# Optimization experiments

Measured on AMD Instinct MI355X. Metric: run time of the kernel, lower is better.

The kernel has to match this reference:

```python
import jax, jax.numpy as jnp
import numpy as np

NEG_SLOPE = 0.2

def gatv2_layer(x, src, dst, Wl, bl, Wr, br, att, bias, N, concat):
    # Wl/Wr: [F_in, H*C]; att: [H, C]
    H, C = att.shape
    xl = (x @ Wl + bl).reshape(-1, H, C)  # source transform [N,H,C]
    xr = (x @ Wr + br).reshape(-1, H, C)  # target transform [N,H,C]
    e = jax.nn.leaky_relu(xl[src] + xr[dst], NEG_SLOPE)          # [E,H,C]
    logits = jnp.einsum('ehc,hc->eh', e, att)                    # [E,H]
    m = jax.ops.segment_max(logits, dst, num_segments=N)         # [N,H]
    p = jnp.exp(logits - m[dst])
    s = jax.ops.segment_sum(p, dst, num_segments=N)              # [N,H]
    alpha = p / s[dst]                                           # [E,H] softmax per dst
    out = jax.ops.segment_sum(alpha[:, :, None] * xl[src], dst, num_segments=N)  # [N,H,C]
    out = out.reshape(N, H * C) if concat else out.mean(axis=1)
    return out + bias


def setup_inputs() -> dict:
    key = jax.random.key(0)
    N, E, F_in = 50000, 500000, 58
    ks = jax.random.split(key, 16)
    s = 0.1
    inp = {
        'x': jax.random.normal(ks[0], (N, F_in), jnp.float32),
        'edge_index': jax.random.randint(ks[1], (2, E), 0, N, jnp.int64),
        'Wl1': jax.random.normal(ks[2], (F_in, 256), jnp.float32) * s,
        'bl1': jnp.zeros((256,), jnp.float32),
        'Wr1': jax.random.normal(ks[3], (F_in, 256), jnp.float32) * s,
        'br1': jnp.zeros((256,), jnp.float32),
        'att1': jax.random.normal(ks[4], (4, 64), jnp.float32) * s,
        'bias1': jnp.zeros((256,), jnp.float32),
        'Wl2': jax.random.normal(ks[5], (256, 256), jnp.float32) * s,
        'bl2': jnp.zeros((256,), jnp.float32),
        'Wr2': jax.random.normal(ks[6], (256, 256), jnp.float32) * s,
        'br2': jnp.zeros((256,), jnp.float32),
        'att2': jax.random.normal(ks[7], (4, 64), jnp.float32) * s,
        'bias2': jnp.zeros((256,), jnp.float32),
        'Wl3': jax.random.normal(ks[8], (256, 6), jnp.float32) * s,
        'bl3': jnp.zeros((6,), jnp.float32),
        'Wr3': jax.random.normal(ks[9], (256, 6), jnp.float32) * s,
        'br3': jnp.zeros((6,), jnp.float32),
        'att3': jax.random.normal(ks[10], (6, 1), jnp.float32) * s,
        'bias3': jnp.zeros((1,), jnp.float32),
    }
    return inp


def reference(x, edge_index, Wl1, bl1, Wr1, br1, att1, bias1,
              Wl2, bl2, Wr2, br2, att2, bias2,
              Wl3, bl3, Wr3, br3, att3, bias3):
    N = x.shape[0]
    loop = jnp.arange(N, dtype=edge_index.dtype)
    src = jnp.concatenate([edge_index[0], loop])  # self-loops (PyG default)
    dst = jnp.concatenate([edge_index[1], loop])
    h = jax.nn.elu(gatv2_layer(x, src, dst, Wl1, bl1, Wr1, br1, att1, bias1, N, True))
    h = jax.nn.elu(gatv2_layer(h, src, dst, Wl2, bl2, Wr2, br2, att2, bias2, N, True))
    out = gatv2_layer(h, src, dst, Wl3, bl3, Wr3, br3, att3, bias3, N, False)
    return out  # [N, 1]
```

## Files before the change

### kernel.cpp

```cpp
#include <hip/hip_runtime.h>
#include <math.h>

#define NEG_SLOPE 0.2f
#define LOG2E 1.4426950408889634f

typedef __attribute__((ext_vector_type(2))) _Float16 h2;
typedef __attribute__((ext_vector_type(4))) _Float16 h4;
typedef __attribute__((ext_vector_type(8))) _Float16 f16x8;
typedef __attribute__((ext_vector_type(4))) float f32x4;

typedef const __attribute__((address_space(1))) unsigned int* gu32p;
typedef __attribute__((address_space(3))) unsigned int* lu32p;

#define GLD16(g, l) __builtin_amdgcn_global_load_lds((gu32p)(g), (lu32p)(l), 16, 0, 0)

template<int CTRL>
__device__ __forceinline__ float dpp_add_f32(float x) {
    int y = __builtin_amdgcn_update_dpp(0, __float_as_int(x), CTRL, 0xF, 0xF, true);
    return x + __int_as_float(y);
}
__device__ __forceinline__ float rowsum16(float x) {
    x = dpp_add_f32<0xB1>(x);
    x = dpp_add_f32<0x4E>(x);
    x = dpp_add_f32<0x124>(x);
    x = dpp_add_f32<0x128>(x);
    return x;
}


__global__ __launch_bounds__(256) void k_scan_block(const int* __restrict__ cnt,
                                                    int* __restrict__ out,
                                                    int* __restrict__ bsums, int n) {
    __shared__ int tmp[256];
    int t = threadIdx.x;
    int i = blockIdx.x * 256 + t;
    int v = (i < n) ? cnt[i] : 0;
    tmp[t] = v;
    __syncthreads();
    for (int d = 1; d < 256; d <<= 1) {
        int add = (t >= d) ? tmp[t - d] : 0;
        __syncthreads();
        tmp[t] += add;
        __syncthreads();
    }
    if (i < n) out[i] = tmp[t] - v;
    if (t == 255) bsums[blockIdx.x] = tmp[t];
}

__global__ __launch_bounds__(256) void k_scan_add(int* __restrict__ out,
                                                  const int* __restrict__ bsums,
                                                  int n, int total, int nb) {
    __shared__ int tmp[256];
    int t = threadIdx.x;
    int v = (t < nb) ? bsums[t] : 0;
    tmp[t] = v;
    __syncthreads();
    for (int d = 1; d < 256; d <<= 1) {
        int add = (t >= d) ? tmp[t - d] : 0;
        __syncthreads();
        tmp[t] += add;
        __syncthreads();
    }
    int boff = tmp[blockIdx.x] - bsums[blockIdx.x];
    int i = blockIdx.x * 256 + t;
    if (i < n) out[i] += boff;
    if (i == 0) out[n] = total;
}


__global__ __launch_bounds__(256) void k_prep(
        const int* __restrict__ ei, int E, int Et, int* __restrict__ cnt,
        int* __restrict__ rank,
        const float* __restrict__ x, _Float16* __restrict__ xb, int N, int F,
        const float* __restrict__ Wl1, const float* __restrict__ Wr1,
        const float* __restrict__ Wl2, const float* __restrict__ Wr2,
        const float* __restrict__ Wl3, const float* __restrict__ Wr3,
        _Float16* __restrict__ wtl1, _Float16* __restrict__ wtr1,
        _Float16* __restrict__ wtl2, _Float16* __restrict__ wtr2,
        _Float16* __restrict__ w3t, int gEt, int gX) {
    const int b = blockIdx.x;
    if (b < gEt) {
        int e = b * 256 + threadIdx.x;
        if (e < Et) {
            int d = (e < E) ? ei[E + e] : (e - E);
            rank[e] = atomicAdd(&cnt[d], 1);
        }
    } else if (b < gEt + gX) {
        int i = (b - gEt) * 256 + threadIdx.x;
        if (i < (N << 6)) {
            int n = i >> 6, k = i & 63;
            xb[i] = (_Float16)(k < F ? x[n * F + k] : 0.0f);
        }
    } else {
        int i = (b - gEt - gX) * 256 + threadIdx.x;
        if (i < 32768) {
            const float* W = (i < 16384) ? Wl1 : Wr1;
            _Float16* O = (i < 16384) ? wtl1 : wtr1;
            int loc = i & 16383;
            int n = loc >> 6, k = loc & 63;
            O[loc] = (_Float16)(k < F ? W[k * 256 + n] : 0.0f);
        } else if (i < 163840) {
            int seg = i - 32768;
            const float* W = (seg < 65536) ? Wl2 : Wr2;
            _Float16* O = (seg < 65536) ? wtl2 : wtr2;
            int loc = seg & 65535;
            int n = loc >> 8, k = loc & 255;
            O[loc] = (_Float16)W[k * 256 + n];
        } else if (i < 167936) {
            int loc = i - 163840;
            int j = loc >> 8, k = loc & 255;
            float v = (j < 6) ? Wl3[k * 6 + j] : ((j < 12) ? Wr3[k * 6 + (j - 6)] : 0.0f);
            w3t[loc] = (_Float16)v;
        }
    }
}


__global__ __launch_bounds__(512) void k_gemm_pair_mfma(
        const _Float16* __restrict__ A, int M, int Kp,
        const _Float16* __restrict__ Btl, const _Float16* __restrict__ Btr,
        const float* __restrict__ bl, const float* __restrict__ br,
        _Float16* __restrict__ Cl, _Float16* __restrict__ Cr,
        const int* __restrict__ ei, int E, int Et,
        const int* __restrict__ row_ptr, const int* __restrict__ rank,
        int* __restrict__ src_sorted,
        int sB, int gX) {
    __shared__ _Float16 As[128 * 32];
    __shared__ _Float16 Bs[256 * 32];
    if (blockIdx.x < sB) {
        int e = blockIdx.x * 512 + threadIdx.x;
        if (e < Et) {
            int s, d;
            if (e < E) { s = ei[e]; d = ei[E + e]; } else { s = d = e - E; }
            src_sorted[row_ptr[d] + rank[e]] = s;
        }
        return;
    }
    const int gb = blockIdx.x - sB;
    const int mat = gb >= gX;
    const int bx  = mat ? gb - gX : gb;
    const int tid = threadIdx.x;
    const int wv = tid >> 6, lane = tid & 63;
    const int wr = wv >> 2, wc = wv & 3;
    const int l15 = lane & 15, l4 = lane >> 4;
    const int row0 = bx * 128;
    const _Float16* Bt = mat ? Btr : Btl;
    const float* bias  = mat ? br  : bl;
    _Float16* C        = mat ? Cr  : Cl;

    const int sr = tid >> 2;
    const int sk = (tid & 3) * 8;
    const _Float16* gA  = A  + (size_t)min(row0 + sr, M - 1) * Kp + sk;
    const _Float16* gB0 = Bt + (size_t)sr * Kp + sk;
    const _Float16* gB1 = Bt + (size_t)(sr + 128) * Kp + sk;
    _Float16* lA  = &As[(wv * 16) * 32];
    _Float16* lB0 = &Bs[(wv * 16) * 32];
    _Float16* lB1 = &Bs[(wv * 16 + 128) * 32];

    f32x4 acc[4][4];
    #pragma unroll
    for (int a = 0; a < 4; a++)
        #pragma unroll
        for (int b = 0; b < 4; b++)
            acc[a][b] = (f32x4){0.f, 0.f, 0.f, 0.f};

    for (int k0 = 0; k0 < Kp; k0 += 32) {
        GLD16(gA + k0, lA);
        GLD16(gB0 + k0, lB0);
        GLD16(gB1 + k0, lB1);
        __syncthreads();
        f16x8 wf[4], xf[4];
        #pragma unroll
        for (int ct = 0; ct < 4; ct++)
            wf[ct] = *(const f16x8*)&Bs[(wc * 64 + ct * 16 + l15) * 32 + l4 * 8];
        #pragma unroll
        for (int nt = 0; nt < 4; nt++)
            xf[nt] = *(const f16x8*)&As[(wr * 64 + nt * 16 + l15) * 32 + l4 * 8];
        #pragma unroll
        for (int ct = 0; ct < 4; ct++)
            #pragma unroll
            for (int nt = 0; nt < 4; nt++)
                acc[ct][nt] = __builtin_amdgcn_mfma_f32_16x16x32_f16(
                    wf[ct], xf[nt], acc[ct][nt], 0, 0, 0);
        __syncthreads();
    }

    float4 bv[4];
    #pragma unroll
    for (int ct = 0; ct < 4; ct++)
        bv[ct] = *(const float4*)&bias[wc * 64 + ct * 16 + l4 * 4];
    #pragma unroll
    for (int nt = 0; nt < 4; nt++) {
        int node = row0 + wr * 64 + nt * 16 + l15;
        if (node < M) {
            #pragma unroll
            for (int ct = 0; ct < 4; ct++) {
                h4 hv = {(_Float16)(acc[ct][nt][0] + bv[ct].x),
                         (_Float16)(acc[ct][nt][1] + bv[ct].y),
                         (_Float16)(acc[ct][nt][2] + bv[ct].z),
                         (_Float16)(acc[ct][nt][3] + bv[ct].w)};
                *(h4*)&C[(size_t)node * 256 + wc * 64 + ct * 16 + l4 * 4] = hv;
            }
        }
    }
}


__global__ __launch_bounds__(256) void k_gemm3_mfma(
        const _Float16* __restrict__ h,
        const _Float16* __restrict__ W3t,
        const float* __restrict__ bl, const float* __restrict__ br,
        _Float16* __restrict__ l3, int N) {
    const int wave = threadIdx.x >> 6, lane = threadIdx.x & 63;
    const int l15 = lane & 15, l4 = lane >> 4;
    const int row0 = blockIdx.x * 64 + wave * 16;
    if (row0 >= N) return;

    f16x8 bfr[8];
    #pragma unroll
    for (int ks = 0; ks < 8; ks++)
        bfr[ks] = *(const f16x8*)&W3t[l15 * 256 + ks * 32 + l4 * 8];

    const int arow = min(row0 + l15, N - 1);
    const size_t abase = (size_t)arow * 256;
    f32x4 acc = (f32x4){0.f, 0.f, 0.f, 0.f};
    #pragma unroll
    for (int ks = 0; ks < 8; ks++) {
        f16x8 af = *(const f16x8*)&h[abase + ks * 32 + l4 * 8];
        acc = __builtin_amdgcn_mfma_f32_16x16x32_f16(af, bfr[ks], acc, 0, 0, 0);
    }
    const float bv = (l15 < 6) ? bl[l15] : ((l15 < 12) ? br[l15 - 6] : 0.0f);
    #pragma unroll
    for (int r = 0; r < 4; r++) {
        int gr = row0 + l4 * 4 + r;
        if (gr < N && l15 < 12)
            l3[(size_t)gr * 16 + l15] = (_Float16)(acc[r] + bv);
    }
}


__global__ __launch_bounds__(256) void k_agg256(const _Float16* __restrict__ xl,
                                                const _Float16* __restrict__ xr,
                                                const int* __restrict__ row_ptr,
                                                const int* __restrict__ src_sorted,
                                                const float* __restrict__ att,
                                                const float* __restrict__ bias,
                                                _Float16* __restrict__ h_out, int N) {
    const int wave = threadIdx.x >> 6;
    const int lane = threadIdx.x & 63;
    const int n = __builtin_amdgcn_readfirstlane(blockIdx.x * 4 + wave);
    if (n >= N) return;
    const int ci = lane * 4;
    const h4 xr4 = *(const h4*)&xr[(size_t)n * 256 + ci];
    const float4 at4 = *(const float4*)&att[ci];
    const h2 ata = {(_Float16)(at4.x * LOG2E), (_Float16)(at4.y * LOG2E)};
    const h2 atb = {(_Float16)(at4.z * LOG2E), (_Float16)(at4.w * LOG2E)};
    h4 a4 = {(_Float16)0.f, (_Float16)0.f, (_Float16)0.f, (_Float16)0.f};
    float m = -INFINITY, s = 0.0f;
    const int beg = row_ptr[n], end = row_ptr[n + 1];
    const int rem = (end - beg) & 7;
    const int tb  = end - rem;

    h4 vt[7];
    #pragma unroll
    for (int e = 0; e < 7; e++) {
        if (e < rem) {
            int sv = src_sorted[tb + e];
            vt[e] = *(const h4*)&xl[(size_t)sv * 256 + ci];
        }
    }

    int j = beg;
    h4 v[8], vn[8];
    bool has = (j + 8 <= tb);
    if (has) {
        #pragma unroll
        for (int e = 0; e < 8; e++) {
            int sv = src_sorted[j + e];
            v[e] = *(const h4*)&xl[(size_t)sv * 256 + ci];
        }
    }
    while (has) {
        const int jn = j + 8;
        const bool hasN = (jn + 8 <= tb);
        if (hasN) {
            #pragma unroll
            for (int e = 0; e < 8; e++) {
                int sv = src_sorted[jn + e];
                vn[e] = *(const h4*)&xl[(size_t)sv * 256 + ci];
            }
        }
        float lg[8];
        #pragma unroll
        for (int e = 0; e < 8; e++) {
            h4 t = v[e] + xr4;
            h4 lk = __builtin_elementwise_max(t, t * (_Float16)NEG_SLOPE);
            h2 lo = __builtin_shufflevector(lk, lk, 0, 1);
            h2 hi = __builtin_shufflevector(lk, lk, 2, 3);
            lg[e] = __builtin_amdgcn_fdot2(lo, ata,
                        __builtin_amdgcn_fdot2(hi, atb, 0.0f, false), false);
        }
        #pragma unroll
        for (int e = 0; e < 8; e++) lg[e] = rowsum16(lg[e]);
        float bm = fmaxf(fmaxf(fmaxf(lg[0], lg[1]), fmaxf(lg[2], lg[3])),
                         fmaxf(fmaxf(lg[4], lg[5]), fmaxf(lg[6], lg[7])));
        float nm = fmaxf(m, bm);
        float sc = __builtin_amdgcn_exp2f(m - nm);
        {
            _Float16 sc16 = (_Float16)sc;
            a4 *= (h4){sc16, sc16, sc16, sc16};
        }
        float ps = 0.f;
        #pragma unroll
        for (int e = 0; e < 8; e++) {
            float p = __builtin_amdgcn_exp2f(lg[e] - nm);
            ps += p;
            _Float16 p16 = (_Float16)p;
            a4 = __builtin_elementwise_fma((h4){p16, p16, p16, p16}, v[e], a4);
        }
        s = s * sc + ps;
        m = nm;
        if (hasN) {
            #pragma unroll
            for (int e = 0; e < 8; e++) v[e] = vn[e];
        }
        j = jn;
        has = hasN;
    }

    if (rem) {
        float lg[7];
        #pragma unroll
        for (int e = 0; e < 7; e++) {
            if (e < rem) {
                h4 t = vt[e] + xr4;
                h4 lk = __builtin_elementwise_max(t, t * (_Float16)NEG_SLOPE);
                h2 lo = __builtin_shufflevector(lk, lk, 0, 1);
                h2 hi = __builtin_shufflevector(lk, lk, 2, 3);
                float d = __builtin_amdgcn_fdot2(lo, ata,
                              __builtin_amdgcn_fdot2(hi, atb, 0.0f, false), false);
                lg[e] = rowsum16(d);
            }
        }
        float bm = -INFINITY;
        #pragma unroll
        for (int e = 0; e < 7; e++)
            if (e < rem) bm = fmaxf(bm, lg[e]);
        float nm = fmaxf(m, bm);
        float sc = __builtin_amdgcn_exp2f(m - nm);
        {
            _Float16 sc16 = (_Float16)sc;
            a4 *= (h4){sc16, sc16, sc16, sc16};
        }
        float ps = 0.f;
        #pragma unroll
        for (int e = 0; e < 7; e++) {
            if (e < rem) {
                float p = __builtin_amdgcn_exp2f(lg[e] - nm);
                ps += p;
                _Float16 p16 = (_Float16)p;
                a4 = __builtin_elementwise_fma((h4){p16, p16, p16, p16}, vt[e], a4);
            }
        }
        s = s * sc + ps;
        m = nm;
    }

    const float inv = 1.0f / s;
    const float4 bv = *(const float4*)&bias[ci];
    float o0 = (float)a4.x * inv + bv.x;
    float o1 = (float)a4.y * inv + bv.y;
    float o2 = (float)a4.z * inv + bv.z;
    float o3 = (float)a4.w * inv + bv.w;
    o0 = o0 > 0.f ? o0 : (__expf(o0) - 1.f);
    o1 = o1 > 0.f ? o1 : (__expf(o1) - 1.f);
    o2 = o2 > 0.f ? o2 : (__expf(o2) - 1.f);
    o3 = o3 > 0.f ? o3 : (__expf(o3) - 1.f);
    h4 hv = {(_Float16)o0, (_Float16)o1, (_Float16)o2, (_Float16)o3};
    *(h4*)&h_out[(size_t)n * 256 + ci] = hv;
}


__global__ __launch_bounds__(256) void k_agg3(const _Float16* __restrict__ l3,
                                              const int* __restrict__ row_ptr,
                                              const int* __restrict__ src_sorted,
                                              const float* __restrict__ att3,
                                              const float* __restrict__ bias3,
                                              float* __restrict__ out, int N) {
    const int idx = blockIdx.x * 256 + threadIdx.x;
    const int n = idx >> 3, h = idx & 7;
    if (n >= N) return;
    float val = 0.0f;
    if (h < 6) {
        const float xrv = (float)l3[(size_t)n * 16 + 6 + h];
        const float attv = att3[h] * LOG2E;
        float m = -INFINITY, s = 0.0f, acc = 0.0f;
        const int beg = row_ptr[n], end = row_ptr[n + 1];
        for (int j = beg; j < end; j += 8) {
            float xlv[8];
            #pragma unroll
            for (int e = 0; e < 8; e++) {
                int i2 = j + e; i2 = i2 < end ? i2 : end - 1;
                int sv = src_sorted[i2];
                xlv[e] = (float)l3[(size_t)sv * 16 + h];
            }
            #pragma unroll
            for (int e = 0; e < 8; e++) {
                const bool valid = (j + e) < end;
                float tt = xlv[e] + xrv;
                float lr = fmaxf(tt, NEG_SLOPE * tt);
                float logit = valid ? (attv * lr) : -INFINITY;
                float nm = fmaxf(m, logit);
                float sc = __builtin_amdgcn_exp2f(m - nm);
                float p  = __builtin_amdgcn_exp2f(logit - nm);
                acc = acc * sc + p * xlv[e];
                s   = s * sc + p;
                m   = nm;
            }
        }
        val = acc / s;
    }
    val += __shfl_xor(val, 1);
    val += __shfl_xor(val, 2);
    val += __shfl_xor(val, 4);
    if (h == 0) out[n] = val * (1.0f / 6.0f) + bias3[0];
}


extern "C" void kernel_launch(void* const* d_in, const int* in_sizes, int n_in,
                              void* d_out, int out_size, void* d_ws, size_t ws_size,
                              hipStream_t stream) {
    const float* x    = (const float*)d_in[0];
    const int*   ei   = (const int*)  d_in[1];
    const float* Wl1  = (const float*)d_in[2];
    const float* bl1  = (const float*)d_in[3];
    const float* Wr1  = (const float*)d_in[4];
    const float* br1  = (const float*)d_in[5];
    const float* att1 = (const float*)d_in[6];
    const float* bias1= (const float*)d_in[7];
    const float* Wl2  = (const float*)d_in[8];
    const float* bl2  = (const float*)d_in[9];
    const float* Wr2  = (const float*)d_in[10];
    const float* br2  = (const float*)d_in[11];
    const float* att2 = (const float*)d_in[12];
    const float* bias2= (const float*)d_in[13];
    const float* Wl3  = (const float*)d_in[14];
    const float* bl3  = (const float*)d_in[15];
    const float* Wr3  = (const float*)d_in[16];
    const float* br3  = (const float*)d_in[17];
    const float* att3 = (const float*)d_in[18];
    const float* bias3= (const float*)d_in[19];

    const int F  = in_sizes[2] / 256;
    const int N  = in_sizes[0] / F;
    const int E  = in_sizes[1] / 2;
    const int Et = E + N;

    char* ws = (char*)d_ws;
    size_t off = 0;
    auto carve = [&](size_t bytes) -> char* {
        char* p = ws + off;
        off = (off + bytes + 255) & ~(size_t)255;
        return p;
    };
    _Float16* xb   = (_Float16*)carve((size_t)N * 64 * 2);
    _Float16* xlb  = (_Float16*)carve((size_t)N * 256 * 2);
    _Float16* xrb  = (_Float16*)carve((size_t)N * 256 * 2);
    _Float16* hb   = (_Float16*)carve((size_t)N * 256 * 2);
    _Float16* wtl1 = (_Float16*)carve(256 * 64 * 2);
    _Float16* wtr1 = (_Float16*)carve(256 * 64 * 2);
    _Float16* wtl2 = (_Float16*)carve(256 * 256 * 2);
    _Float16* wtr2 = (_Float16*)carve(256 * 256 * 2);
    _Float16* w3t  = (_Float16*)carve(16 * 256 * 2);
    _Float16* l3   = (_Float16*)carve((size_t)N * 16 * 2);
    int* cnt        = (int*)carve((size_t)N * 4);
    int* row_ptr    = (int*)carve((size_t)(N + 1) * 4);
    int* rank       = (int*)carve((size_t)Et * 4);
    int* src_sorted = (int*)carve((size_t)Et * 4);
    int* bsums      = (int*)carve(1024 * 4);

    const int gN  = (N + 255) / 256;
    const int gEt = (Et + 255) / 256;
    const int gX  = ((N << 6) + 255) / 256;
    const int gW  = (N + 3) / 4;
    const int gx1 = (N + 127) / 128;
    const int sB  = (Et + 511) / 512;

    hipMemsetAsync(cnt, 0, (size_t)N * 4, stream);
    k_prep<<<gEt + gX + 656, 256, 0, stream>>>(ei, E, Et, cnt, rank, x, xb, N, F,
                                               Wl1, Wr1, Wl2, Wr2, Wl3, Wr3,
                                               wtl1, wtr1, wtl2, wtr2, w3t, gEt, gX);

    k_scan_block<<<gN, 256, 0, stream>>>(cnt, row_ptr, bsums, N);
    k_scan_add<<<gN, 256, 0, stream>>>(row_ptr, bsums, N, Et, gN);

    k_gemm_pair_mfma<<<sB + 2 * gx1, 512, 0, stream>>>(
        xb, N, 64, wtl1, wtr1, bl1, br1, xlb, xrb,
        ei, E, Et, row_ptr, rank, src_sorted, sB, gx1);
    k_agg256<<<gW, 256, 0, stream>>>(xlb, xrb, row_ptr, src_sorted, att1, bias1, hb, N);

    k_gemm_pair_mfma<<<2 * gx1, 512, 0, stream>>>(
        hb, N, 256, wtl2, wtr2, bl2, br2, xlb, xrb,
        ei, E, Et, row_ptr, rank, src_sorted, 0, gx1);
    k_agg256<<<gW, 256, 0, stream>>>(xlb, xrb, row_ptr, src_sorted, att2, bias2, hb, N);

    k_gemm3_mfma<<<(N + 63) / 64, 256, 0, stream>>>(hb, w3t, bl3, br3, l3, N);
    k_agg3<<<((N * 8) + 255) / 256, 256, 0, stream>>>(l3, row_ptr, src_sorted, att3, bias3,
                                                      (float*)d_out, N);
}
```

Baseline: 296.8 us.

## Fuse left and right GEMMs into one 1024-thread block sharing the A tile

The paired GEMM kernel now computes both the Wl and Wr projections in a single 1024-thread block, with waves 0-7 handling the left matrix and waves 8-15 the right. Each shared A tile is loaded once and reused for both outputs, halving A traffic and halving the grid size. The edge-scatter prologue blocks are resized to 1024 threads to match. The cost is that a larger block under launch bounds of 1024 limits registers per thread and lowers scheduling flexibility, and LDS per block grows.

```diff
diff --git a/kernel.cpp b/kernel.cpp
--- a/kernel.cpp
+++ b/kernel.cpp
@@ -116,7 +116,7 @@
 }
 
 
-__global__ __launch_bounds__(512) void k_gemm_pair_mfma(
+__global__ __launch_bounds__(1024) void k_gemm_pair_mfma(
         const _Float16* __restrict__ A, int M, int Kp,
         const _Float16* __restrict__ Btl, const _Float16* __restrict__ Btr,
         const float* __restrict__ bl, const float* __restrict__ br,
@@ -124,11 +124,12 @@
         const int* __restrict__ ei, int E, int Et,
         const int* __restrict__ row_ptr, const int* __restrict__ rank,
         int* __restrict__ src_sorted,
-        int sB, int gX) {
-    __shared__ _Float16 As[128 * 32];
-    __shared__ _Float16 Bs[256 * 32];
+        int sB) {
+    __shared__ _Float16 As [128 * 32];
+    __shared__ _Float16 Bs0[256 * 32];
+    __shared__ _Float16 Bs1[256 * 32];
     if (blockIdx.x < sB) {
-        int e = blockIdx.x * 512 + threadIdx.x;
+        int e = blockIdx.x * 1024 + threadIdx.x;
         if (e < Et) {
             int s, d;
             if (e < E) { s = ei[e]; d = ei[E + e]; } else { s = d = e - E; }
@@ -136,26 +137,26 @@
         }
         return;
     }
-    const int gb = blockIdx.x - sB;
-    const int mat = gb >= gX;
-    const int bx  = mat ? gb - gX : gb;
+    const int bx  = blockIdx.x - sB;
     const int tid = threadIdx.x;
     const int wv = tid >> 6, lane = tid & 63;
-    const int wr = wv >> 2, wc = wv & 3;
+    const int mat = wv >> 3;
+    const int wq  = wv & 7;
+    const int wr = wq >> 2, wc = wq & 3;
     const int l15 = lane & 15, l4 = lane >> 4;
     const int row0 = bx * 128;
-    const _Float16* Bt = mat ? Btr : Btl;
     const float* bias  = mat ? br  : bl;
     _Float16* C        = mat ? Cr  : Cl;
 
     const int sr = tid >> 2;
     const int sk = (tid & 3) * 8;
-    const _Float16* gA  = A  + (size_t)min(row0 + sr, M - 1) * Kp + sk;
-    const _Float16* gB0 = Bt + (size_t)sr * Kp + sk;
-    const _Float16* gB1 = Bt + (size_t)(sr + 128) * Kp + sk;
-    _Float16* lA  = &As[(wv * 16) * 32];
-    _Float16* lB0 = &Bs[(wv * 16) * 32];
-    _Float16* lB1 = &Bs[(wv * 16 + 128) * 32];
+    const _Float16* gA  = A   + (size_t)min(row0 + sr, M - 1) * Kp + sk;
+    const _Float16* gB0 = Btl + (size_t)sr * Kp + sk;
+    const _Float16* gB1 = Btr + (size_t)sr * Kp + sk;
+    _Float16* lA  = &As [(wv * 16) * 32];
+    _Float16* lB0 = &Bs0[(wv * 16) * 32];
+    _Float16* lB1 = &Bs1[(wv * 16) * 32];
+    const _Float16* Bs = mat ? Bs1 : Bs0;
 
     f32x4 acc[4][4];
     #pragma unroll
@@ -165,7 +166,7 @@
             acc[a][b] = (f32x4){0.f, 0.f, 0.f, 0.f};
 
     for (int k0 = 0; k0 < Kp; k0 += 32) {
-        GLD16(gA + k0, lA);
+        if (wv < 8) GLD16(gA + k0, lA);
         GLD16(gB0 + k0, lB0);
         GLD16(gB1 + k0, lB1);
         __syncthreads();
@@ -484,7 +485,7 @@
     const int gX  = ((N << 6) + 255) / 256;
     const int gW  = (N + 3) / 4;
     const int gx1 = (N + 127) / 128;
-    const int sB  = (Et + 511) / 512;
+    const int sB  = (Et + 1023) / 1024;
 
     hipMemsetAsync(cnt, 0, (size_t)N * 4, stream);
     k_prep<<<gEt + gX + 656, 256, 0, stream>>>(ei, E, Et, cnt, rank, x, xb, N, F,
@@ -494,14 +495,14 @@
     k_scan_block<<<gN, 256, 0, stream>>>(cnt, row_ptr, bsums, N);
     k_scan_add<<<gN, 256, 0, stream>>>(row_ptr, bsums, N, Et, gN);
 
-    k_gemm_pair_mfma<<<sB + 2 * gx1, 512, 0, stream>>>(
+    k_gemm_pair_mfma<<<sB + gx1, 1024, 0, stream>>>(
         xb, N, 64, wtl1, wtr1, bl1, br1, xlb, xrb,
-        ei, E, Et, row_ptr, rank, src_sorted, sB, gx1);
+        ei, E, Et, row_ptr, rank, src_sorted, sB);
     k_agg256<<<gW, 256, 0, stream>>>(xlb, xrb, row_ptr, src_sorted, att1, bias1, hb, N);
 
-    k_gemm_pair_mfma<<<2 * gx1, 512, 0, stream>>>(
+    k_gemm_pair_mfma<<<gx1, 1024, 0, stream>>>(
         hb, N, 256, wtl2, wtr2, bl2, br2, xlb, xrb,
-        ei, E, Et, row_ptr, rank, src_sorted, 0, gx1);
+        ei, E, Et, row_ptr, rank, src_sorted, 0);
     k_agg256<<<gW, 256, 0, stream>>>(xlb, xrb, row_ptr, src_sorted, att2, bias2, hb, N);
 
     k_gemm3_mfma<<<(N + 63) / 64, 256, 0, stream>>>(hb, w3t, bl3, br3, l3, N);
```

Result: slower. 306.9 us (+3.4%).
